# Kernel optimization log

Measured on AMD Instinct MI355X. Metric: run time of the kernel, lower is better.

Reference implementation:

```python
import jax, jax.numpy as jnp
import numpy as np

N = 100000
E = 3200000
IN_DIM = 768
HID = 128
NUM_CLASSES = 7


def gcn_conv(x, W, b, src, dst, n):
    """PyG GCNConv: h = D^-1/2 (A+I) D^-1/2 (x W) + b, symmetric normalization."""
    h = x @ W  # [n, out]
    loop = jnp.arange(n, dtype=src.dtype)
    s = jnp.concatenate([src, loop])  # sources (messages flow src -> dst)
    d = jnp.concatenate([dst, loop])
    deg = jax.ops.segment_sum(jnp.ones(s.shape[0], dtype=h.dtype), d, num_segments=n)
    dinv = jnp.where(deg > 0, jax.lax.rsqrt(deg), 0.0)
    norm = dinv[s] * dinv[d]  # [E+n]
    msgs = h[s] * norm[:, None]
    out = jax.ops.segment_sum(msgs, d, num_segments=n)
    return out + b


def setup_inputs() -> dict:
    key = jax.random.key(0)
    ks = jax.random.split(key, 8)
    x = jax.random.normal(ks[0], (N, IN_DIM), dtype=jnp.float32)
    edge_index = jax.random.randint(ks[1], (2, E), 0, N, dtype=jnp.int32)
    W1 = jax.random.normal(ks[2], (IN_DIM, HID), dtype=jnp.float32) / np.sqrt(IN_DIM)
    b1 = jnp.zeros((HID,), dtype=jnp.float32)
    W2 = jax.random.normal(ks[3], (HID, HID), dtype=jnp.float32) / np.sqrt(HID)
    b2 = jnp.zeros((HID,), dtype=jnp.float32)
    Wc = jax.random.normal(ks[4], (HID, NUM_CLASSES), dtype=jnp.float32) / np.sqrt(HID)
    bc = jnp.zeros((NUM_CLASSES,), dtype=jnp.float32)
    return {"x": x, "edge_index": edge_index, "W1": W1, "b1": b1,
            "W2": W2, "b2": b2, "Wc": Wc, "bc": bc}


def reference(x, edge_index, W1, b1, W2, b2, Wc, bc):
    src, dst = edge_index[0], edge_index[1]
    n = x.shape[0]
    h = jax.nn.relu(gcn_conv(x, W1, b1, src, dst, n))
    h = jax.nn.relu(gcn_conv(h, W2, b2, src, dst, n))
    logits = h @ Wc + bc
    return logits
```

## Files before the change

### kernel.cpp

```cpp
#include <hip/hip_runtime.h>
#include <hip/hip_bf16.h>

#define IN_DIM 768
#define HID 128
#define NC 7

typedef __attribute__((ext_vector_type(8))) short bf16x8;
typedef __attribute__((ext_vector_type(4))) float f32x4;

__device__ __forceinline__ ushort f2bf(float f) {
  uint u = __float_as_uint(f);
  u += 0x7fffu + ((u >> 16) & 1u);
  return (ushort)(u >> 16);
}
__device__ __forceinline__ float lof(uint v) { return __uint_as_float(v << 16); }
__device__ __forceinline__ float hif(uint v) { return __uint_as_float(v & 0xffff0000u); }
__device__ __forceinline__ uint cvtpk(float lo, float hi) {
  uint r;
  asm("v_cvt_pk_bf16_f32 %0, %1, %2" : "=v"(r) : "v"(lo), "v"(hi));
  return r;
}


__global__ __launch_bounds__(256) void k_count(const int* __restrict__ dst,
                                               int* __restrict__ cnt,
                                               int* __restrict__ pos, int E) {
  int e0 = (blockIdx.x * 256 + threadIdx.x) * 4;
  if (e0 + 4 <= E) {
    int4 d = *(const int4*)&dst[e0];
    int4 p;
    p.x = atomicAdd(&cnt[d.x], 1);
    p.y = atomicAdd(&cnt[d.y], 1);
    p.z = atomicAdd(&cnt[d.z], 1);
    p.w = atomicAdd(&cnt[d.w], 1);
    *(int4*)&pos[e0] = p;
  } else {
    for (int e = e0; e < E; ++e) pos[e] = atomicAdd(&cnt[dst[e]], 1);
  }
}

__device__ __forceinline__ int pad4(int c) { return (c + 3) & ~3; }

__global__ void k_scan_partial(const int* __restrict__ cnt, int* __restrict__ partials, int N) {
  __shared__ int sm[256];
  int b = blockIdx.x, t = threadIdx.x;
  int base = b * 1024 + t * 4;
  int s = 0;
  #pragma unroll
  for (int j = 0; j < 4; ++j) if (base + j < N) s += pad4(cnt[base + j]);
  sm[t] = s;
  __syncthreads();
  for (int off = 128; off > 0; off >>= 1) {
    if (t < off) sm[t] += sm[t + off];
    __syncthreads();
  }
  if (t == 0) partials[b] = sm[0];
}

__global__ void k_scan_combine(int* __restrict__ partials, int* __restrict__ rowptr,
                               int nch, int N) {
  __shared__ int sm[128];
  int t = threadIdx.x;
  int v0 = (t < nch) ? partials[t] : 0;
  sm[t] = v0;
  __syncthreads();
  for (int off = 1; off < 128; off <<= 1) {
    int add = (t >= off) ? sm[t - off] : 0;
    __syncthreads();
    sm[t] += add;
    __syncthreads();
  }
  if (t < nch) partials[t] = sm[t] - v0;
  if (t == 0) rowptr[N] = sm[127];
}

__global__ void k_scan_final(const int* __restrict__ cnt, const int* __restrict__ chunkoff,
                             int* __restrict__ rowptr, int N) {
  __shared__ int sm[256];
  int b = blockIdx.x, t = threadIdx.x;
  int base = b * 1024 + t * 4;
  int v[4]; int s = 0;
  #pragma unroll
  for (int j = 0; j < 4; ++j) { v[j] = (base + j < N) ? pad4(cnt[base + j]) : 0; s += v[j]; }
  sm[t] = s;
  __syncthreads();
  for (int off = 1; off < 256; off <<= 1) {
    int add = (t >= off) ? sm[t - off] : 0;
    __syncthreads();
    sm[t] += add;
    __syncthreads();
  }
  int excl = sm[t] - s;
  int run = chunkoff[b] + excl;
  #pragma unroll
  for (int j = 0; j < 4; ++j) {
    if (base + j < N) rowptr[base + j] = run;
    run += v[j];
  }
}

__global__ void k_dinv(const int* __restrict__ cnt, float* __restrict__ dinv, int N) {
  int n = blockIdx.x * 256 + threadIdx.x;
  if (n < N) dinv[n] = rsqrtf((float)(cnt[n] + 1));
}

__global__ void k_fill(int* __restrict__ p, int val, int total) {
  int i = (blockIdx.x * 256 + threadIdx.x) * 4;
  if (i + 4 <= total) {
    *(int4*)&p[i] = make_int4(val, val, val, val);
  } else {
    for (; i < total; ++i) p[i] = val;
  }
}

__global__ __launch_bounds__(256)
void k_scatter(const int* __restrict__ src, const int* __restrict__ dst,
               const int* __restrict__ pos, const int* __restrict__ rowptr,
               int* __restrict__ srcs, int E) {
  int e0 = (blockIdx.x * 256 + threadIdx.x) * 8;
  if (e0 + 8 <= E) {
    int s[8], d[8], p[8];
    *(int4*)&s[0] = *(const int4*)&src[e0];
    *(int4*)&s[4] = *(const int4*)&src[e0 + 4];
    *(int4*)&d[0] = *(const int4*)&dst[e0];
    *(int4*)&d[4] = *(const int4*)&dst[e0 + 4];
    *(int4*)&p[0] = *(const int4*)&pos[e0];
    *(int4*)&p[4] = *(const int4*)&pos[e0 + 4];
    int rp[8];
    #pragma unroll
    for (int j = 0; j < 8; ++j) rp[j] = rowptr[d[j]];
    #pragma unroll
    for (int j = 0; j < 8; ++j) srcs[rp[j] + p[j]] = s[j];
  } else {
    for (int e = e0; e < E; ++e) srcs[rowptr[dst[e]] + pos[e]] = src[e];
  }
}

__global__ void k_convW(const float* __restrict__ W, ushort* __restrict__ WT, int K) {
  int i = blockIdx.x * 256 + threadIdx.x;
  if (i >= K * HID) return;
  int k = i >> 7, c = i & 127;
  WT[c * K + k] = f2bf(W[i]);
}

__global__ __launch_bounds__(256)
void k_gemm1(const float* __restrict__ A, const ushort* __restrict__ WT,
             const float* __restrict__ dinv, ushort* __restrict__ G, const int N) {
  __shared__ ushort lB[2][128 * 64];
  const int tid = threadIdx.x;
  const int lane = tid & 63;
  const int wid = tid >> 6;
  const int lr = lane & 15, lq = lane >> 4;
  const int rb = blockIdx.x * 128 + wid * 16;
  int ar0 = rb + lr;      if (ar0 > N - 1) ar0 = N - 1;
  int ar1 = rb + 64 + lr; if (ar1 > N - 1) ar1 = N - 1;
  const float* Ap0 = A + (size_t)ar0 * IN_DIM + lq * 8;
  const float* Ap1 = A + (size_t)ar1 * IN_DIM + lq * 8;

  auto stageB = [&](int buf, int k0) {
    #pragma unroll
    for (int j = 0; j < 4; ++j) {
      int i = j * 256 + tid;
      int r = i >> 3;
      int c = ((i & 7) ^ (r & 7)) * 8;
      __builtin_amdgcn_global_load_lds((const uint*)(WT + (size_t)r * IN_DIM + k0 + c),
                                       (uint*)&lB[buf][i * 8], 16, 0, 0);
    }
  };

  float4 fa0[4], fa1[4];
  auto loadA = [&](int k0) {
    const float* p0 = Ap0 + k0;
    fa0[0] = *(const float4*)p0;
    fa0[1] = *(const float4*)(p0 + 4);
    fa0[2] = *(const float4*)(p0 + 32);
    fa0[3] = *(const float4*)(p0 + 36);
    const float* p1 = Ap1 + k0;
    fa1[0] = *(const float4*)p1;
    fa1[1] = *(const float4*)(p1 + 4);
    fa1[2] = *(const float4*)(p1 + 32);
    fa1[3] = *(const float4*)(p1 + 36);
  };

  f32x4 acc0[8], acc1[8];
  #pragma unroll
  for (int n = 0; n < 8; ++n) {
    acc0[n] = (f32x4){0.f, 0.f, 0.f, 0.f};
    acc1[n] = (f32x4){0.f, 0.f, 0.f, 0.f};
  }

  loadA(0);
  stageB(0, 0);
  __syncthreads();

  constexpr int NT = IN_DIM / 64;
  for (int t = 0; t < NT; ++t) {
    const int cur = t & 1;
    bf16x8 av0[2], av1[2];
    {
      uint* u = (uint*)&av0[0];
      u[0] = cvtpk(fa0[0].x, fa0[0].y); u[1] = cvtpk(fa0[0].z, fa0[0].w);
      u[2] = cvtpk(fa0[1].x, fa0[1].y); u[3] = cvtpk(fa0[1].z, fa0[1].w);
      u[4] = cvtpk(fa0[2].x, fa0[2].y); u[5] = cvtpk(fa0[2].z, fa0[2].w);
      u[6] = cvtpk(fa0[3].x, fa0[3].y); u[7] = cvtpk(fa0[3].z, fa0[3].w);
      uint* v = (uint*)&av1[0];
      v[0] = cvtpk(fa1[0].x, fa1[0].y); v[1] = cvtpk(fa1[0].z, fa1[0].w);
      v[2] = cvtpk(fa1[1].x, fa1[1].y); v[3] = cvtpk(fa1[1].z, fa1[1].w);
      v[4] = cvtpk(fa1[2].x, fa1[2].y); v[5] = cvtpk(fa1[2].z, fa1[2].w);
      v[6] = cvtpk(fa1[3].x, fa1[3].y); v[7] = cvtpk(fa1[3].z, fa1[3].w);
    }
    if (t + 1 < NT) { loadA((t + 1) * 64); stageB(cur ^ 1, (t + 1) * 64); }
    #pragma unroll
    for (int kk = 0; kk < 2; ++kk) {
      #pragma unroll
      for (int n = 0; n < 8; ++n) {
        int C = n * 16 + lr;
        int slot = (kk * 4 + lq) ^ (C & 7);
        bf16x8 bv = *(const bf16x8*)&lB[cur][C * 64 + slot * 8];
        acc0[n] = __builtin_amdgcn_mfma_f32_16x16x32_bf16(av0[kk], bv, acc0[n], 0, 0, 0);
        acc1[n] = __builtin_amdgcn_mfma_f32_16x16x32_bf16(av1[kk], bv, acc1[n], 0, 0, 0);
      }
    }
    __syncthreads();
  }

  #pragma unroll
  for (int i = 0; i < 4; ++i) {
    int row0 = rb + lq * 4 + i;
    int row1 = rb + 64 + lq * 4 + i;
    float dv0 = (row0 < N) ? dinv[row0] : 0.f;
    float dv1 = (row1 < N) ? dinv[row1] : 0.f;
    #pragma unroll
    for (int n = 0; n < 8; ++n) {
      if (row0 < N) G[(size_t)row0 * HID + n * 16 + lr] = f2bf(dv0 * acc0[n][i]);
      if (row1 < N) G[(size_t)row1 * HID + n * 16 + lr] = f2bf(dv1 * acc1[n][i]);
    }
  }
}

__global__ __launch_bounds__(256)
void k_gemm2(const ushort* __restrict__ A, const ushort* __restrict__ WT,
             const float* __restrict__ dinv, ushort* __restrict__ G, const int N) {
  __shared__ ushort lA[2][128 * 64];
  __shared__ ushort lB[2][128 * 64];
  const int tid = threadIdx.x;
  const int lane = tid & 63;
  const int wid = tid >> 6;
  const int wm = wid >> 1, wn = wid & 1;
  const int row0 = blockIdx.x * 128;
  const int lr = lane & 15;
  const int lk8 = lane >> 4;
  constexpr int K = HID;

  auto stage = [&](int buf, int k0) {
    #pragma unroll
    for (int j = 0; j < 4; ++j) {
      int i = j * 256 + tid;
      int r = i >> 3;
      int c = ((i & 7) ^ (r & 7)) * 8;
      int ga = row0 + r; ga = ga < N ? ga : N - 1;
      __builtin_amdgcn_global_load_lds((const uint*)(A + (size_t)ga * K + k0 + c),
                                       (uint*)&lA[buf][i * 8], 16, 0, 0);
      __builtin_amdgcn_global_load_lds((const uint*)(WT + (size_t)r * K + k0 + c),
                                       (uint*)&lB[buf][i * 8], 16, 0, 0);
    }
  };

  f32x4 acc[4][4];
  #pragma unroll
  for (int m = 0; m < 4; ++m)
    #pragma unroll
    for (int n = 0; n < 4; ++n)
      acc[m][n] = (f32x4){0.f, 0.f, 0.f, 0.f};

  constexpr int NT = K / 64;
  stage(0, 0);
  __syncthreads();

  for (int t = 0; t < NT; ++t) {
    const int cur = t & 1;
    if (t + 1 < NT) stage(cur ^ 1, (t + 1) * 64);
    #pragma unroll
    for (int kk = 0; kk < 2; ++kk) {
      bf16x8 av[4], bv[4];
      #pragma unroll
      for (int m = 0; m < 4; ++m) {
        int R = wm * 64 + m * 16 + lr;
        int slot = (kk * 4 + lk8) ^ (R & 7);
        av[m] = *(const bf16x8*)&lA[cur][R * 64 + slot * 8];
      }
      #pragma unroll
      for (int n = 0; n < 4; ++n) {
        int C = wn * 64 + n * 16 + lr;
        int slot = (kk * 4 + lk8) ^ (C & 7);
        bv[n] = *(const bf16x8*)&lB[cur][C * 64 + slot * 8];
      }
      #pragma unroll
      for (int m = 0; m < 4; ++m)
        #pragma unroll
        for (int n = 0; n < 4; ++n)
          acc[m][n] = __builtin_amdgcn_mfma_f32_16x16x32_bf16(av[m], bv[n], acc[m][n], 0, 0, 0);
    }
    __syncthreads();
  }

  #pragma unroll
  for (int m = 0; m < 4; ++m) {
    #pragma unroll
    for (int i = 0; i < 4; ++i) {
      int row = row0 + wm * 64 + m * 16 + (lane >> 4) * 4 + i;
      if (row < N) {
        float dv = dinv[row];
        #pragma unroll
        for (int n = 0; n < 4; ++n) {
          int col = wn * 64 + n * 16 + lr;
          G[(size_t)row * HID + col] = f2bf(dv * acc[m][n][i]);
        }
      }
    }
  }
}


#define GL(v, s) uint v = Gp[(size_t)(s) * 64 + lane];
#define AC(v) { a0 += lof(v); a1 += hif(v); }

__device__ __forceinline__ void agg32(const uint* __restrict__ Gp,
                                      const int* __restrict__ srcs,
                                      int i, int lane, float& a0, float& a1) {
  int4 sa = *(const int4*)&srcs[i];
  int4 sb = *(const int4*)&srcs[i + 4];
  int4 sc = *(const int4*)&srcs[i + 8];
  int4 sd = *(const int4*)&srcs[i + 12];
  int4 se = *(const int4*)&srcs[i + 16];
  int4 sf = *(const int4*)&srcs[i + 20];
  int4 sg = *(const int4*)&srcs[i + 24];
  int4 sh = *(const int4*)&srcs[i + 28];
  GL(h00, sa.x) GL(h01, sa.y) GL(h02, sa.z) GL(h03, sa.w)
  GL(h04, sb.x) GL(h05, sb.y) GL(h06, sb.z) GL(h07, sb.w)
  GL(h08, sc.x) GL(h09, sc.y) GL(h10, sc.z) GL(h11, sc.w)
  GL(h12, sd.x) GL(h13, sd.y) GL(h14, sd.z) GL(h15, sd.w)
  GL(h16, se.x) GL(h17, se.y) GL(h18, se.z) GL(h19, se.w)
  GL(h20, sf.x) GL(h21, sf.y) GL(h22, sf.z) GL(h23, sf.w)
  GL(h24, sg.x) GL(h25, sg.y) GL(h26, sg.z) GL(h27, sg.w)
  GL(h28, sh.x) GL(h29, sh.y) GL(h30, sh.z) GL(h31, sh.w)
  __builtin_amdgcn_sched_barrier(0);
  AC(h00) AC(h01) AC(h02) AC(h03) AC(h04) AC(h05) AC(h06) AC(h07)
  AC(h08) AC(h09) AC(h10) AC(h11) AC(h12) AC(h13) AC(h14) AC(h15)
  AC(h16) AC(h17) AC(h18) AC(h19) AC(h20) AC(h21) AC(h22) AC(h23)
  AC(h24) AC(h25) AC(h26) AC(h27) AC(h28) AC(h29) AC(h30) AC(h31)
}

__device__ __forceinline__ void agg16(const uint* __restrict__ Gp,
                                      const int* __restrict__ srcs,
                                      int i, int lane, float& a0, float& a1) {
  int4 sa = *(const int4*)&srcs[i];
  int4 sb = *(const int4*)&srcs[i + 4];
  int4 sc = *(const int4*)&srcs[i + 8];
  int4 sd = *(const int4*)&srcs[i + 12];
  GL(h00, sa.x) GL(h01, sa.y) GL(h02, sa.z) GL(h03, sa.w)
  GL(h04, sb.x) GL(h05, sb.y) GL(h06, sb.z) GL(h07, sb.w)
  GL(h08, sc.x) GL(h09, sc.y) GL(h10, sc.z) GL(h11, sc.w)
  GL(h12, sd.x) GL(h13, sd.y) GL(h14, sd.z) GL(h15, sd.w)
  __builtin_amdgcn_sched_barrier(0);
  AC(h00) AC(h01) AC(h02) AC(h03) AC(h04) AC(h05) AC(h06) AC(h07)
  AC(h08) AC(h09) AC(h10) AC(h11) AC(h12) AC(h13) AC(h14) AC(h15)
}

__device__ __forceinline__ void agg4(const uint* __restrict__ Gp,
                                     const int* __restrict__ srcs,
                                     int i, int lane, float& a0, float& a1) {
  int4 sa = *(const int4*)&srcs[i];
  GL(h00, sa.x) GL(h01, sa.y) GL(h02, sa.z) GL(h03, sa.w)
  __builtin_amdgcn_sched_barrier(0);
  AC(h00) AC(h01) AC(h02) AC(h03)
}

__global__ __launch_bounds__(256)
void k_agg(const uint* __restrict__ Gp, const int* __restrict__ srcs,
           const int* __restrict__ rowptr, const float* __restrict__ dinv,
           const float* __restrict__ bias, uint* __restrict__ Ou, int N) {
  int w = (blockIdx.x * 256 + threadIdx.x) >> 6;
  if (w >= N) return;
  int lane = threadIdx.x & 63;
  int start = rowptr[w], end = rowptr[w + 1];
  float di = dinv[w];
  uint hv = Gp[(size_t)w * 64 + lane];
  float a0 = lof(hv), a1 = hif(hv);
  int i = start;
  for (; i + 32 <= end; i += 32) agg32(Gp, srcs, i, lane, a0, a1);
  for (; i + 16 <= end; i += 16) agg16(Gp, srcs, i, lane, a0, a1);
  for (; i < end; i += 4)        agg4(Gp, srcs, i, lane, a0, a1);
  float2 bb = ((const float2*)bias)[lane];
  a0 = fmaxf(fmaf(di, a0, bb.x), 0.f);
  a1 = fmaxf(fmaf(di, a1, bb.y), 0.f);
  Ou[(size_t)w * 64 + lane] = (uint)f2bf(a0) | ((uint)f2bf(a1) << 16);
}

__global__ __launch_bounds__(256)
void k_agg_final(const uint* __restrict__ Gp, const int* __restrict__ srcs,
                 const int* __restrict__ rowptr, const float* __restrict__ dinv,
                 const float* __restrict__ bias, const float* __restrict__ Wc,
                 const float* __restrict__ bc, float* __restrict__ out, int N) {
  int w = (blockIdx.x * 256 + threadIdx.x) >> 6;
  if (w >= N) return;
  int lane = threadIdx.x & 63;
  int start = rowptr[w], end = rowptr[w + 1];
  float di = dinv[w];
  uint hv = Gp[(size_t)w * 64 + lane];
  float a0 = lof(hv), a1 = hif(hv);
  int i = start;
  for (; i + 32 <= end; i += 32) agg32(Gp, srcs, i, lane, a0, a1);
  for (; i + 16 <= end; i += 16) agg16(Gp, srcs, i, lane, a0, a1);
  for (; i < end; i += 4)        agg4(Gp, srcs, i, lane, a0, a1);
  float2 bb = ((const float2*)bias)[lane];
  a0 = fmaxf(fmaf(di, a0, bb.x), 0.f);
  a1 = fmaxf(fmaf(di, a1, bb.y), 0.f);
  const float* w0 = &Wc[(2 * lane) * NC];
  #pragma unroll
  for (int c = 0; c < NC; ++c) {
    float s = a0 * w0[c] + a1 * w0[NC + c];
    #pragma unroll
    for (int off = 32; off > 0; off >>= 1) s += __shfl_xor(s, off, 64);
    if (lane == 0) out[(size_t)w * NC + c] = s + bc[c];
  }
}

extern "C" void kernel_launch(void* const* d_in, const int* in_sizes, int n_in,
                              void* d_out, int out_size, void* d_ws, size_t ws_size,
                              hipStream_t stream) {
  const float* x  = (const float*)d_in[0];
  const int*   ei = (const int*)d_in[1];
  const float* W1 = (const float*)d_in[2];
  const float* b1 = (const float*)d_in[3];
  const float* W2 = (const float*)d_in[4];
  const float* b2 = (const float*)d_in[5];
  const float* Wc = (const float*)d_in[6];
  const float* bc = (const float*)d_in[7];
  float* out = (float*)d_out;

  const int N = in_sizes[0] / IN_DIM;
  const int E = in_sizes[1] / 2;
  const int* src = ei;
  const int* dst = ei + E;
  const int CSRCAP = E + 3 * N + 64;

  char* ws = (char*)d_ws;
  size_t off = 0;
  auto alloc = [&](size_t bytes) -> void* {
    off = (off + 255) & ~(size_t)255;
    void* p = ws + off;
    off += bytes;
    return p;
  };
  ushort* H0     = (ushort*)alloc((size_t)(N + 1) * HID * 2);
  ushort* H1     = (ushort*)alloc((size_t)(N + 1) * HID * 2);
  int*    srcs   = (int*)alloc((size_t)CSRCAP * 4);
  int*    cnt    = (int*)alloc((size_t)N * 4);
  int*    pos    = (int*)alloc((size_t)E * 4);
  int*    rowptr = (int*)alloc((size_t)(N + 1) * 4);
  float*  dinv   = (float*)alloc((size_t)N * 4);
  int*    partials = (int*)alloc(512);
  ushort* W1T    = (ushort*)alloc((size_t)IN_DIM * HID * 2);
  ushort* W2T    = (ushort*)alloc((size_t)HID * HID * 2);

  hipMemsetAsync(cnt, 0, (size_t)N * 4, stream);
  hipMemsetAsync(H0 + (size_t)N * HID, 0, HID * 2, stream);

  k_convW<<<(IN_DIM * HID + 255) / 256, 256, 0, stream>>>(W1, W1T, IN_DIM);
  k_convW<<<(HID * HID + 255) / 256, 256, 0, stream>>>(W2, W2T, HID);

  k_count<<<(E + 1023) / 1024, 256, 0, stream>>>(dst, cnt, pos, E);
  int nch = (N + 1023) >> 10;
  k_scan_partial<<<nch, 256, 0, stream>>>(cnt, partials, N);
  k_scan_combine<<<1, 128, 0, stream>>>(partials, rowptr, nch, N);
  k_scan_final<<<nch, 256, 0, stream>>>(cnt, partials, rowptr, N);
  k_dinv<<<(N + 255) / 256, 256, 0, stream>>>(cnt, dinv, N);
  k_fill<<<(CSRCAP + 1023) / 1024, 256, 0, stream>>>(srcs, N, CSRCAP);
  k_scatter<<<(E + 2047) / 2048, 256, 0, stream>>>(src, dst, pos, rowptr, srcs, E);

  k_gemm1<<<(N + 127) / 128, 256, 0, stream>>>(x, W1T, dinv, H0, N);
  k_agg<<<(N + 3) / 4, 256, 0, stream>>>((const uint*)H0, srcs, rowptr, dinv, b1,
                                         (uint*)H1, N);
  k_gemm2<<<(N + 127) / 128, 256, 0, stream>>>(H1, W2T, dinv, H0, N);
  k_agg_final<<<(N + 3) / 4, 256, 0, stream>>>((const uint*)H0, srcs, rowptr, dinv, b2,
                                               Wc, bc, out, N);
}
```

Baseline: 587.3 us.

## Fuse gemm1, CSR scatter and padding fill into one interleaved launch

Merges the layer-1 GEMM, the edge scatter into CSR, and a per-row padding fill into one kernel whose blocks are interleaved by slot, so the memory-bound scatter overlaps the compute-bound GEMM. The full-buffer fill of the CSR array is replaced by writing the sentinel only into each row's padding tail. This removes two launches and a large memset-like pass, but every block now reserves the GEMM's shared memory, which may lower occupancy for the scatter blocks.

```diff
diff --git a/kernel.cpp b/kernel.cpp
--- a/kernel.cpp
+++ b/kernel.cpp
@@ -104,38 +104,6 @@
   if (n < N) dinv[n] = rsqrtf((float)(cnt[n] + 1));
 }
 
-__global__ void k_fill(int* __restrict__ p, int val, int total) {
-  int i = (blockIdx.x * 256 + threadIdx.x) * 4;
-  if (i + 4 <= total) {
-    *(int4*)&p[i] = make_int4(val, val, val, val);
-  } else {
-    for (; i < total; ++i) p[i] = val;
-  }
-}
-
-__global__ __launch_bounds__(256)
-void k_scatter(const int* __restrict__ src, const int* __restrict__ dst,
-               const int* __restrict__ pos, const int* __restrict__ rowptr,
-               int* __restrict__ srcs, int E) {
-  int e0 = (blockIdx.x * 256 + threadIdx.x) * 8;
-  if (e0 + 8 <= E) {
-    int s[8], d[8], p[8];
-    *(int4*)&s[0] = *(const int4*)&src[e0];
-    *(int4*)&s[4] = *(const int4*)&src[e0 + 4];
-    *(int4*)&d[0] = *(const int4*)&dst[e0];
-    *(int4*)&d[4] = *(const int4*)&dst[e0 + 4];
-    *(int4*)&p[0] = *(const int4*)&pos[e0];
-    *(int4*)&p[4] = *(const int4*)&pos[e0 + 4];
-    int rp[8];
-    #pragma unroll
-    for (int j = 0; j < 8; ++j) rp[j] = rowptr[d[j]];
-    #pragma unroll
-    for (int j = 0; j < 8; ++j) srcs[rp[j] + p[j]] = s[j];
-  } else {
-    for (int e = e0; e < E; ++e) srcs[rowptr[dst[e]] + pos[e]] = src[e];
-  }
-}
-
 __global__ void k_convW(const float* __restrict__ W, ushort* __restrict__ WT, int K) {
   int i = blockIdx.x * 256 + threadIdx.x;
   if (i >= K * HID) return;
@@ -143,15 +111,17 @@
   WT[c * K + k] = f2bf(W[i]);
 }
 
-__global__ __launch_bounds__(256)
-void k_gemm1(const float* __restrict__ A, const ushort* __restrict__ WT,
-             const float* __restrict__ dinv, ushort* __restrict__ G, const int N) {
-  __shared__ ushort lB[2][128 * 64];
+
+__device__ __forceinline__
+void gemm1_body(ushort (*lB)[128 * 64],
+                const float* __restrict__ A, const ushort* __restrict__ WT,
+                const float* __restrict__ dinv, ushort* __restrict__ G,
+                const int N, int b) {
   const int tid = threadIdx.x;
   const int lane = tid & 63;
   const int wid = tid >> 6;
   const int lr = lane & 15, lq = lane >> 4;
-  const int rb = blockIdx.x * 128 + wid * 16;
+  const int rb = b * 128 + wid * 16;
   int ar0 = rb + lr;      if (ar0 > N - 1) ar0 = N - 1;
   int ar1 = rb + 64 + lr; if (ar1 > N - 1) ar1 = N - 1;
   const float* Ap0 = A + (size_t)ar0 * IN_DIM + lq * 8;
@@ -235,6 +205,61 @@
       if (row0 < N) G[(size_t)row0 * HID + n * 16 + lr] = f2bf(dv0 * acc0[n][i]);
       if (row1 < N) G[(size_t)row1 * HID + n * 16 + lr] = f2bf(dv1 * acc1[n][i]);
     }
+  }
+}
+
+__device__ __forceinline__
+void scatter_body(const int* __restrict__ src, const int* __restrict__ dst,
+                  const int* __restrict__ pos, const int* __restrict__ rowptr,
+                  int* __restrict__ srcs, int E, int b) {
+  int e0 = (b * 256 + threadIdx.x) * 8;
+  if (e0 + 8 <= E) {
+    int s[8], d[8], p[8];
+    *(int4*)&s[0] = *(const int4*)&src[e0];
+    *(int4*)&s[4] = *(const int4*)&src[e0 + 4];
+    *(int4*)&d[0] = *(const int4*)&dst[e0];
+    *(int4*)&d[4] = *(const int4*)&dst[e0 + 4];
+    *(int4*)&p[0] = *(const int4*)&pos[e0];
+    *(int4*)&p[4] = *(const int4*)&pos[e0 + 4];
+    int rp[8];
+    #pragma unroll
+    for (int j = 0; j < 8; ++j) rp[j] = rowptr[d[j]];
+    #pragma unroll
+    for (int j = 0; j < 8; ++j) srcs[rp[j] + p[j]] = s[j];
+  } else {
+    for (int e = e0; e < E; ++e) srcs[rowptr[dst[e]] + pos[e]] = src[e];
+  }
+}
+
+__device__ __forceinline__
+void fillpad_body(const int* __restrict__ cnt, const int* __restrict__ rowptr,
+                  int* __restrict__ srcs, int N, int b) {
+  int n = b * 256 + threadIdx.x;
+  if (n < N) {
+    int c = cnt[n];
+    int e0 = rowptr[n] + c;
+    int e1 = rowptr[n] + pad4(c);
+    for (int i = e0; i < e1; ++i) srcs[i] = N;
+  }
+}
+
+__global__ __launch_bounds__(256)
+void k_mega(const float* __restrict__ A, const ushort* __restrict__ WT,
+            const float* __restrict__ dinv, ushort* __restrict__ G, int N,
+            const int* __restrict__ src, const int* __restrict__ dst,
+            const int* __restrict__ pos, const int* __restrict__ rowptr,
+            int* __restrict__ srcs, int E, const int* __restrict__ cnt,
+            int Gg1, int Gsc, int Gfp) {
+  __shared__ ushort lB[2][128 * 64];
+  int grp = blockIdx.x / 7, slot = blockIdx.x % 7;
+  if (slot < 2) {
+    int b = grp * 2 + slot;
+    if (b < Gg1) gemm1_body(lB, A, WT, dinv, G, N, b);
+  } else if (slot < 6) {
+    int b = grp * 4 + (slot - 2);
+    if (b < Gsc) scatter_body(src, dst, pos, rowptr, srcs, E, b);
+  } else {
+    if (grp < Gfp) fillpad_body(cnt, rowptr, srcs, N, grp);
   }
 }
 
@@ -476,10 +501,17 @@
   k_scan_combine<<<1, 128, 0, stream>>>(partials, rowptr, nch, N);
   k_scan_final<<<nch, 256, 0, stream>>>(cnt, partials, rowptr, N);
   k_dinv<<<(N + 255) / 256, 256, 0, stream>>>(cnt, dinv, N);
-  k_fill<<<(CSRCAP + 1023) / 1024, 256, 0, stream>>>(srcs, N, CSRCAP);
-  k_scatter<<<(E + 2047) / 2048, 256, 0, stream>>>(src, dst, pos, rowptr, srcs, E);
-
-  k_gemm1<<<(N + 127) / 128, 256, 0, stream>>>(x, W1T, dinv, H0, N);
+
+  const int Gg1 = (N + 127) / 128;
+  const int Gsc = (E + 2047) / 2048;
+  const int Gfp = (N + 255) / 256;
+  int ngroups = (Gg1 + 1) / 2;
+  if ((Gsc + 3) / 4 > ngroups) ngroups = (Gsc + 3) / 4;
+  if (Gfp > ngroups) ngroups = Gfp;
+  k_mega<<<ngroups * 7, 256, 0, stream>>>(x, W1T, dinv, H0, N,
+                                          src, dst, pos, rowptr, srcs, E, cnt,
+                                          Gg1, Gsc, Gfp);
+
   k_agg<<<(N + 3) / 4, 256, 0, stream>>>((const uint*)H0, srcs, rowptr, dinv, b1,
                                          (uint*)H1, N);
   k_gemm2<<<(N + 127) / 128, 256, 0, stream>>>(H1, W2T, dinv, H0, N);
```

Result: faster. 565.4 us, median of 2 (-3.7%).
